# Optimization experiments

Hardware: AMD Instinct MI355X
Metric: run time of the kernel (lower is better)

Reference implementation:

```python
import jax, jax.numpy as jnp
import numpy as np

D_MODEL = 1024
NUM_HEADS = 16
ROPE_THETA = 10000.0


def setup_inputs() -> dict:
    key = jax.random.key(0)
    ks = jax.random.split(key, 5)
    B, S, D = 4, 2048, D_MODEL
    scale = 1.0 / np.sqrt(D)
    return {
        "x": jax.random.normal(ks[0], (B, S, D), dtype=jnp.float32),
        "Wq": jax.random.normal(ks[1], (D, D), dtype=jnp.float32) * scale,
        "Wk": jax.random.normal(ks[2], (D, D), dtype=jnp.float32) * scale,
        "Wv": jax.random.normal(ks[3], (D, D), dtype=jnp.float32) * scale,
        "Wo": jax.random.normal(ks[4], (D, D), dtype=jnp.float32) * scale,
        "token_positions": jnp.arange(S, dtype=jnp.int32),
    }


def _rope(x, pos, theta=ROPE_THETA):
    # x: (b, h, s, d); interleaved-pair rotary embedding
    d = x.shape[-1]
    inv_freq = 1.0 / (theta ** (jnp.arange(0, d, 2, dtype=jnp.float32) / d))  # (d/2,)
    ang = pos.astype(jnp.float32)[:, None] * inv_freq[None, :]  # (s, d/2)
    cos, sin = jnp.cos(ang), jnp.sin(ang)
    x1, x2 = x[..., ::2], x[..., 1::2]
    out = jnp.stack([x1 * cos - x2 * sin, x1 * sin + x2 * cos], axis=-1)
    return out.reshape(x.shape)


def reference(x, Wq, Wk, Wv, Wo, token_positions):
    B, S, D = x.shape
    H = NUM_HEADS
    dh = D // H
    # torch nn.Linear(bias=False): y = x @ W.T
    q = jnp.einsum('bsd,ed->bse', x, Wq).reshape(B, S, H, dh).transpose(0, 2, 1, 3)
    k = jnp.einsum('bsd,ed->bse', x, Wk).reshape(B, S, H, dh).transpose(0, 2, 1, 3)
    v = jnp.einsum('bsd,ed->bse', x, Wv).reshape(B, S, H, dh).transpose(0, 2, 1, 3)
    q = _rope(q, token_positions)
    k = _rope(k, token_positions)
    scores = jnp.einsum('bhqd,bhkd->bhqk', q, k) / jnp.sqrt(jnp.array(dh, x.dtype))
    causal = jnp.tril(jnp.ones((S, S), dtype=bool))
    scores = jnp.where(causal, scores, jnp.array(-jnp.inf, scores.dtype))
    probs = jax.nn.softmax(scores, axis=-1)
    attn = jnp.einsum('bhqk,bhkd->bhqd', probs, v)  # (b, h, s, dh)
    attn = attn.transpose(0, 2, 1, 3).reshape(B, S, D)
    return jnp.einsum('bsd,ed->bse', attn, Wo)
```

## Files before the change

### kernel.cpp

```cpp
#include <hip/hip_runtime.h>
#include <hip/hip_bf16.h>
#include <stdint.h>

#define S_LEN 2048
#define BATCH 4
#define NH    16
#define DH    64
#define DM    1024
#define MTOT  (BATCH*S_LEN)

typedef short bf16x8 __attribute__((ext_vector_type(8)));
typedef float f32x4 __attribute__((ext_vector_type(4)));
typedef uint32_t u32x4 __attribute__((ext_vector_type(4)));

__device__ __forceinline__ uint16_t f2bf(float f) {
  union { float f; uint32_t i; } c; c.f = f;
  uint32_t r = c.i + 0x7fffu + ((c.i >> 16) & 1u);
  return (uint16_t)(r >> 16);
}
__device__ __forceinline__ float bf2f(uint16_t u) {
  union { uint32_t i; float f; } c; c.i = ((uint32_t)u) << 16; return c.f;
}

__device__ __forceinline__ uint32_t cvt_pk_bf16(float a, float b) {
  uint32_t r;
  asm("v_cvt_pk_bf16_f32 %0, %1, %2" : "=v"(r) : "v"(a), "v"(b));
  return r;
}

__device__ __forceinline__ void async_copy16(void* lds, const void* g) {
  __builtin_amdgcn_global_load_lds(
      (const __attribute__((address_space(1))) void*)g,
      (__attribute__((address_space(3))) void*)lds, 16, 0, 0);
}

__global__ __launch_bounds__(256) void cvt_f32_bf16(const float* __restrict__ in,
                                                    uint16_t* __restrict__ out, int n4) {
  int stride = gridDim.x * blockDim.x;
  for (int i = blockIdx.x * blockDim.x + threadIdx.x; i < n4; i += stride) {
    float4 v = ((const float4*)in)[i];
    ushort4 o;
    o.x = f2bf(v.x); o.y = f2bf(v.y); o.z = f2bf(v.z); o.w = f2bf(v.w);
    ((ushort4*)out)[i] = o;
  }
}

__global__ __launch_bounds__(256) void cvt_w4(const float* __restrict__ wq,
                                              const float* __restrict__ wk,
                                              const float* __restrict__ wv,
                                              const float* __restrict__ wo,
                                              uint16_t* __restrict__ out) {
  const int sel = blockIdx.y;
  const float* src = sel == 0 ? wq : sel == 1 ? wk : sel == 2 ? wv : wo;
  uint16_t* dst = out + (size_t)sel * DM * DM;
  const int n4 = DM * DM / 4;
  const int stride = gridDim.x * blockDim.x;
  for (int i = blockIdx.x * blockDim.x + threadIdx.x; i < n4; i += stride) {
    float4 v = ((const float4*)src)[i];
    ushort4 o;
    o.x = f2bf(v.x); o.y = f2bf(v.y); o.z = f2bf(v.z); o.w = f2bf(v.w);
    ((ushort4*)dst)[i] = o;
  }
}

template<int MODE>
__global__ __launch_bounds__(256) void gemm_bt(const uint16_t* __restrict__ A,
                                               const uint16_t* __restrict__ Bw,
                                               void* __restrict__ outp) {
  constexpr int K = DM;
  constexpr int NT = K / 32;
  __shared__ __align__(16) uint16_t lA[3][128 * 32];
  __shared__ __align__(16) uint16_t lB[3][128 * 32];
  const int tid = threadIdx.x;
  const int w = tid >> 6, lane = tid & 63;
  const int l15 = lane & 15, lhi = lane >> 4;
  const int wr = w >> 1, wc = w & 1;

  const int nx = gridDim.x, nwg = nx * gridDim.y;
  const int flat = blockIdx.y * nx + blockIdx.x;
  const int wg = (flat & 7) * (nwg >> 3) + (flat >> 3);
  const int bm = (wg / nx) * 128, bn = (wg % nx) * 128;

  const int srow = tid >> 2;
  const int cb = (tid & 3) * 16;

  auto stage = [&](int b, int t) {
    const int k0 = t * 32;
#pragma unroll
    for (int i = 0; i < 2; ++i) {
      const int row = i * 64 + srow;
      async_copy16((char*)lA[b] + i * 4096 + w * 1024,
                   (const char*)A + ((size_t)(bm + row) * K + k0) * 2 + cb);
      async_copy16((char*)lB[b] + i * 4096 + w * 1024,
                   (const char*)Bw + ((size_t)(bn + row) * K + k0) * 2 + cb);
    }
  };

  f32x4 acc[4][4] = {};

  stage(0, 0);
  stage(1, 1);
  asm volatile("s_waitcnt vmcnt(4)" ::: "memory");
  __builtin_amdgcn_s_barrier();
  __builtin_amdgcn_sched_barrier(0);

  int cur = 0;
  for (int t = 0; t < NT; ++t) {
    const bool pre = (t + 2 < NT);
    int bnext = cur + 2; if (bnext >= 3) bnext -= 3;
    if (pre) stage(bnext, t + 2);

    bf16x8 af[4], bfr[4];
#pragma unroll
    for (int mf = 0; mf < 4; ++mf)
      af[mf] = *(const bf16x8*)((const char*)lA[cur] +
                                (wr * 64 + mf * 16 + l15) * 64 + lhi * 16);
#pragma unroll
    for (int nf = 0; nf < 4; ++nf)
      bfr[nf] = *(const bf16x8*)((const char*)lB[cur] +
                                 (wc * 64 + nf * 16 + l15) * 64 + lhi * 16);
    __builtin_amdgcn_s_setprio(1);
#pragma unroll
    for (int mf = 0; mf < 4; ++mf)
#pragma unroll
      for (int nf = 0; nf < 4; ++nf)
        acc[mf][nf] = __builtin_amdgcn_mfma_f32_16x16x32_bf16(af[mf], bfr[nf], acc[mf][nf], 0, 0, 0);
    __builtin_amdgcn_s_setprio(0);

    if (pre) asm volatile("s_waitcnt vmcnt(4)" ::: "memory");
    else     asm volatile("s_waitcnt vmcnt(0)" ::: "memory");
    __builtin_amdgcn_s_barrier();
    __builtin_amdgcn_sched_barrier(0);
    cur = cur + 1 == 3 ? 0 : cur + 1;
  }

  if (MODE == 0) {
    uint16_t* out = (uint16_t*)outp;
#pragma unroll
    for (int mf = 0; mf < 4; ++mf)
#pragma unroll
      for (int nf = 0; nf < 4; ++nf)
#pragma unroll
        for (int r = 0; r < 4; ++r) {
          const int m = bm + wr * 64 + mf * 16 + lhi * 4 + r;
          const int n = bn + wc * 64 + nf * 16 + l15;
          const int b = m >> 11, s = m & (S_LEN - 1);
          const int tsel = n >> 10, e = n & 1023;
          const int h = e >> 6, d = e & 63;
          out[(size_t)tsel * (MTOT * DM) +
              (((size_t)(b * NH + h) * S_LEN + s) << 6) + d] = f2bf(acc[mf][nf][r]);
        }
  } else {
    float* out = (float*)outp;
#pragma unroll
    for (int mf = 0; mf < 4; ++mf)
#pragma unroll
      for (int nf = 0; nf < 4; ++nf)
#pragma unroll
        for (int r = 0; r < 4; ++r) {
          const int m = bm + wr * 64 + mf * 16 + lhi * 4 + r;
          const int n = bn + wc * 64 + nf * 16 + l15;
          out[(size_t)m * DM + n] = acc[mf][nf][r];
        }
  }
}

__global__ __launch_bounds__(256) void rope_kernel(uint32_t* __restrict__ q,
                                                   uint32_t* __restrict__ k,
                                                   const int* __restrict__ pos) {
  const int total = BATCH * NH * S_LEN * 32;
  const float l2t = 13.287712379549449f;
  const float qsc = 0.18033688011112042f;
  const int stride = gridDim.x * blockDim.x;
  for (int idx = blockIdx.x * blockDim.x + threadIdx.x; idx < total; idx += stride) {
    const int i = idx & 31;
    const int s = (idx >> 5) & (S_LEN - 1);
    const float p = (float)pos[s];
    const float inv = __builtin_amdgcn_exp2f(-(float)i * (l2t * (1.0f / 32.0f)));
    const float ang = p * inv;
    const float sn = sinf(ang), cs = cosf(ang);
    {
      uint32_t u = q[idx];
      float x1 = bf2f((uint16_t)(u & 0xffffu));
      float x2 = bf2f((uint16_t)(u >> 16));
      q[idx] = (uint32_t)f2bf((x1 * cs - x2 * sn) * qsc) |
               ((uint32_t)f2bf((x1 * sn + x2 * cs) * qsc) << 16);
    }
    {
      uint32_t u = k[idx];
      float x1 = bf2f((uint16_t)(u & 0xffffu));
      float x2 = bf2f((uint16_t)(u >> 16));
      k[idx] = (uint32_t)f2bf(x1 * cs - x2 * sn) | ((uint32_t)f2bf(x1 * sn + x2 * cs) << 16);
    }
  }
}

__global__ __launch_bounds__(256) void transpose_v(const uint16_t* __restrict__ v,
                                                   uint16_t* __restrict__ vt) {
  __shared__ uint16_t t[64 * 65];
  const int bh = blockIdx.y, s0 = blockIdx.x * 64;
  const uint16_t* vb = v + (size_t)bh * S_LEN * 64 + (size_t)s0 * 64;
  uint16_t* ob = vt + (size_t)bh * 64 * S_LEN + s0;
  for (int o = threadIdx.x; o < 64 * 64; o += 256) {
    const int r = o >> 6, c = o & 63;
    t[c * 65 + r] = vb[(size_t)r * 64 + c];
  }
  __syncthreads();
  for (int o = threadIdx.x; o < 64 * 64; o += 256) {
    const int d = o >> 6, p = o & 63;
    const int sp = (p & 32) | (((p >> 2) & 3) << 3) | (((p >> 4) & 1) << 2) | (p & 3);
    ob[(size_t)d * S_LEN + sp] = t[d * 65 + p];
  }
}

__global__ __launch_bounds__(512, 4) void attn_kernel(const uint16_t* __restrict__ q,
                                                      const uint16_t* __restrict__ kk,
                                                      const uint16_t* __restrict__ vt,
                                                      uint16_t* __restrict__ o) {
  const int bh = blockIdx.y;
  const int p = blockIdx.x;
  const int tid = threadIdx.x;
  const int w = __builtin_amdgcn_readfirstlane(tid >> 6);
  const int lane = tid & 63;
  const int l15 = lane & 15, lhi = lane >> 4;
  const uint16_t* qb = q + (size_t)bh * S_LEN * DH;
  const uint16_t* kb = kk + (size_t)bh * S_LEN * DH;
  const uint16_t* vb = vt + (size_t)bh * DH * S_LEN;

  __shared__ uint16_t lK[2][128 * 64];
  __shared__ uint16_t lV[2][64 * 128];

  const int krow_l = lane >> 3;
  const int scK = (lane & 7) ^ krow_l;
  const int vrow_l = lane >> 4;

  auto stage = [&](int b, int t) {
    const int k0 = t * 128;
#pragma unroll
    for (int i = 0; i < 2; ++i) {
      const int krow = w * 16 + i * 8 + krow_l;
      async_copy16((char*)lK[b] + w * 2048 + i * 1024 + lane * 16,
                   (const char*)kb + ((size_t)(k0 + krow) * 64 + scK * 8) * 2);
      const int vd = w * 8 + i * 4 + vrow_l;
      const int scV = (lane & 15) ^ (vd & 15);
      async_copy16((char*)lV[b] + w * 2048 + i * 1024 + lane * 16,
                   (const char*)vb + ((size_t)vd * S_LEN + k0 + scV * 8) * 2);
    }
  };

  stage(0, 0);
  asm volatile("s_waitcnt vmcnt(0)" ::: "memory");
  __syncthreads();

  int cur = 0;
  const int b_out = bh >> 4, h_out = bh & 15;

  for (int s = 0; s < 2; ++s) {
    const int qtile = s ? p : (15 - p);
    const int q0 = qtile * 128 + w * 16;

    bf16x8 qf[2];
#pragma unroll
    for (int c = 0; c < 2; ++c)
      qf[c] = *(const bf16x8*)(qb + (size_t)(q0 + l15) * DH + c * 32 + lhi * 8);

    f32x4 oa[4] = {};
    float mr = -1e30f, lr = 0.f;

    const int nt = qtile + 1;
    for (int t = 0; t < nt; ++t) {
      if (t + 1 < nt) stage(cur ^ 1, t + 1);
      else if (s == 0) stage(cur ^ 1, 0);

      const bool diag = (t == qtile);
      const int fMf = diag ? w : 7;
      const int fE  = diag ? (w | 1) : 7;
      const int cE  = diag ? (w >> 1) : 3;

      f32x4 sf[8];
      __builtin_amdgcn_s_setprio(1);
#pragma unroll
      for (int f = 0; f < 8; ++f) {
        f32x4 z = {0.f, 0.f, 0.f, 0.f};
        if (f <= fMf) {
          const int kr = f * 16 + l15;
          const char* kbase = (const char*)lK[cur] + kr * 128;
          bf16x8 kf0 = *(const bf16x8*)(kbase + ((lhi ^ (kr & 7)) << 4));
          bf16x8 kf1 = *(const bf16x8*)(kbase + (((4 + lhi) ^ (kr & 7)) << 4));
          z = __builtin_amdgcn_mfma_f32_16x16x32_bf16(kf0, qf[0], z, 0, 0, 0);
          z = __builtin_amdgcn_mfma_f32_16x16x32_bf16(kf1, qf[1], z, 0, 0, 0);
        }
        sf[f] = z;
      }
      __builtin_amdgcn_s_setprio(0);

      if (diag) {
        const int qrow = q0 + l15;
        const int k0 = t * 128;
#pragma unroll
        for (int f = 0; f < 8; ++f)
          if (f <= fE)
#pragma unroll
            for (int r = 0; r < 4; ++r) {
              const int kv = k0 + f * 16 + lhi * 4 + r;
              if (kv > qrow) sf[f][r] = -1e30f;
            }
      }

      float pm = -1e30f;
#pragma unroll
      for (int f = 0; f < 8; ++f)
        if (f <= fE)
#pragma unroll
          for (int r = 0; r < 4; ++r) pm = fmaxf(pm, sf[f][r]);
      pm = fmaxf(pm, __shfl_xor(pm, 16));
      pm = fmaxf(pm, __shfl_xor(pm, 32));

      if (!__all(pm <= mr + 8.0f)) {
        const float mn = fmaxf(mr, pm);
        const float resc = __builtin_amdgcn_exp2f(mr - mn);
        mr = mn;
        lr *= resc;
#pragma unroll
        for (int r = 0; r < 4; ++r) {
          const float rb = __shfl(resc, (lhi << 2) + r);
#pragma unroll
          for (int df = 0; df < 4; ++df) oa[df][r] *= rb;
        }
      }

      float rs = 0.f;
#pragma unroll
      for (int f = 0; f < 8; ++f)
        if (f <= fE)
#pragma unroll
          for (int r = 0; r < 4; ++r) {
            const float pv = __builtin_amdgcn_exp2f(sf[f][r] - mr);
            sf[f][r] = pv;
            rs += pv;
          }
      rs += __shfl_xor(rs, 16);
      rs += __shfl_xor(rs, 32);
      lr += rs;

#pragma unroll
      for (int c = 0; c < 4; ++c) {
        if (c <= cE) {
          u32x4 u;
          u.x = cvt_pk_bf16(sf[2 * c][0], sf[2 * c][1]);
          u.y = cvt_pk_bf16(sf[2 * c][2], sf[2 * c][3]);
          u.z = cvt_pk_bf16(sf[2 * c + 1][0], sf[2 * c + 1][1]);
          u.w = cvt_pk_bf16(sf[2 * c + 1][2], sf[2 * c + 1][3]);
          bf16x8 pa = __builtin_bit_cast(bf16x8, u);
          __builtin_amdgcn_s_setprio(1);
#pragma unroll
          for (int df = 0; df < 4; ++df) {
            const int vr = df * 16 + l15;
            bf16x8 vf = *(const bf16x8*)((const char*)lV[cur] + vr * 256 +
                                         ((((c << 2) + lhi) ^ (vr & 15)) << 4));
            oa[df] = __builtin_amdgcn_mfma_f32_16x16x32_bf16(pa, vf, oa[df], 0, 0, 0);
          }
          __builtin_amdgcn_s_setprio(0);
        }
      }

      asm volatile("s_waitcnt vmcnt(0)" ::: "memory");
      __syncthreads();
      cur ^= 1;
    }

    float inv[4];
#pragma unroll
    for (int r = 0; r < 4; ++r)
      inv[r] = __builtin_amdgcn_rcpf(__shfl(lr, (lhi << 2) + r));
#pragma unroll
    for (int df = 0; df < 4; ++df)
#pragma unroll
      for (int r = 0; r < 4; ++r) {
        const int srow_o = q0 + lhi * 4 + r;
        const float val = oa[df][r] * inv[r];
        const int d = df * 16 + l15;
        o[((size_t)(b_out * S_LEN + srow_o)) * DM + h_out * 64 + d] = f2bf(val);
      }
  }
}

extern "C" void kernel_launch(void* const* d_in, const int* in_sizes, int n_in,
                              void* d_out, int out_size, void* d_ws, size_t ws_size,
                              hipStream_t stream) {
  const float* x = (const float*)d_in[0];
  const float* Wq = (const float*)d_in[1];
  const float* Wk = (const float*)d_in[2];
  const float* Wv = (const float*)d_in[3];
  const float* Wo = (const float*)d_in[4];
  const int* pos = (const int*)d_in[5];

  char* ws = (char*)d_ws;
  size_t off = 0;
  auto alloc = [&](size_t bytes) {
    void* p = ws + off;
    off += (bytes + 255) & ~(size_t)255;
    return p;
  };
  uint16_t* xb    = (uint16_t*)alloc((size_t)MTOT * DM * 2);
  uint16_t* wqkvb = (uint16_t*)alloc((size_t)4 * DM * DM * 2);
  uint16_t* qkvb  = (uint16_t*)alloc((size_t)3 * MTOT * DM * 2);
  uint16_t* vtb   = (uint16_t*)alloc((size_t)MTOT * DM * 2);
  uint16_t* wob = wqkvb + (size_t)3 * DM * DM;
  uint16_t* qb = qkvb;
  uint16_t* kbuf = qkvb + (size_t)MTOT * DM;
  uint16_t* vbuf = qkvb + (size_t)2 * MTOT * DM;
  uint16_t* attnb = xb;

  cvt_f32_bf16<<<2048, 256, 0, stream>>>(x, xb, MTOT * DM / 4);
  cvt_w4<<<dim3(128, 4), 256, 0, stream>>>(Wq, Wk, Wv, Wo, wqkvb);

  gemm_bt<0><<<dim3(24, MTOT / 128), 256, 0, stream>>>(xb, wqkvb, qkvb);

  rope_kernel<<<2048, 256, 0, stream>>>((uint32_t*)qb, (uint32_t*)kbuf, pos);
  transpose_v<<<dim3(32, 64), 256, 0, stream>>>(vbuf, vtb);

  attn_kernel<<<dim3(8, 64), 512, 0, stream>>>(qb, kbuf, vtb, attnb);

  gemm_bt<1><<<dim3(8, MTOT / 128), 256, 0, stream>>>(attnb, wob, d_out);
}
```

Baseline: 187.5 us.

## Fuse RoPE into QKV GEMM epilogue and narrow output-projection tile

RoPE rotation and the query scaling now happen in the QKV GEMM epilogue. Each lane takes its pair element from a neighbour lane with a shuffle, which removes the separate rope kernel and its extra read-modify-write of Q and K. The GEMM is templated on the N tile width. The output projection uses BN=64, doubling its workgroup count from 512 to 1024 for better CU occupancy. The risks are per-element transcendental cost in the epilogue (__sinf/__cosf instead of sinf/cosf, lower accuracy at large angles) and less reuse per tile in the narrower projection GEMM.

```diff
diff --git a/kernel.cpp b/kernel.cpp
--- a/kernel.cpp
+++ b/kernel.cpp
@@ -63,14 +63,17 @@
   }
 }
 
-template<int MODE>
+template<int MODE, int BN>
 __global__ __launch_bounds__(256) void gemm_bt(const uint16_t* __restrict__ A,
                                                const uint16_t* __restrict__ Bw,
-                                               void* __restrict__ outp) {
+                                               void* __restrict__ outp,
+                                               const int* __restrict__ pos) {
   constexpr int K = DM;
   constexpr int NT = K / 32;
+  constexpr int WC = BN / 2;
+  constexpr int NF = WC / 16;
   __shared__ __align__(16) uint16_t lA[3][128 * 32];
-  __shared__ __align__(16) uint16_t lB[3][128 * 32];
+  __shared__ __align__(16) uint16_t lB[3][BN * 32];
   const int tid = threadIdx.x;
   const int w = tid >> 6, lane = tid & 63;
   const int l15 = lane & 15, lhi = lane >> 4;
@@ -79,7 +82,7 @@
   const int nx = gridDim.x, nwg = nx * gridDim.y;
   const int flat = blockIdx.y * nx + blockIdx.x;
   const int wg = (flat & 7) * (nwg >> 3) + (flat >> 3);
-  const int bm = (wg / nx) * 128, bn = (wg % nx) * 128;
+  const int bm = (wg / nx) * 128, bn = (wg % nx) * BN;
 
   const int srow = tid >> 2;
   const int cb = (tid & 3) * 16;
@@ -87,20 +90,21 @@
   auto stage = [&](int b, int t) {
     const int k0 = t * 32;
 #pragma unroll
-    for (int i = 0; i < 2; ++i) {
-      const int row = i * 64 + srow;
+    for (int i = 0; i < 2; ++i)
       async_copy16((char*)lA[b] + i * 4096 + w * 1024,
-                   (const char*)A + ((size_t)(bm + row) * K + k0) * 2 + cb);
+                   (const char*)A + ((size_t)(bm + i * 64 + srow) * K + k0) * 2 + cb);
+#pragma unroll
+    for (int i = 0; i < BN / 64; ++i)
       async_copy16((char*)lB[b] + i * 4096 + w * 1024,
-                   (const char*)Bw + ((size_t)(bn + row) * K + k0) * 2 + cb);
-    }
+                   (const char*)Bw + ((size_t)(bn + i * 64 + srow) * K + k0) * 2 + cb);
   };
 
-  f32x4 acc[4][4] = {};
+  f32x4 acc[4][NF] = {};
 
   stage(0, 0);
   stage(1, 1);
-  asm volatile("s_waitcnt vmcnt(4)" ::: "memory");
+  if constexpr (BN == 128) asm volatile("s_waitcnt vmcnt(4)" ::: "memory");
+  else                     asm volatile("s_waitcnt vmcnt(3)" ::: "memory");
   __builtin_amdgcn_s_barrier();
   __builtin_amdgcn_sched_barrier(0);
 
@@ -110,88 +114,94 @@
     int bnext = cur + 2; if (bnext >= 3) bnext -= 3;
     if (pre) stage(bnext, t + 2);
 
-    bf16x8 af[4], bfr[4];
+    bf16x8 af[4], bfr[NF];
 #pragma unroll
     for (int mf = 0; mf < 4; ++mf)
       af[mf] = *(const bf16x8*)((const char*)lA[cur] +
                                 (wr * 64 + mf * 16 + l15) * 64 + lhi * 16);
 #pragma unroll
-    for (int nf = 0; nf < 4; ++nf)
+    for (int nf = 0; nf < NF; ++nf)
       bfr[nf] = *(const bf16x8*)((const char*)lB[cur] +
-                                 (wc * 64 + nf * 16 + l15) * 64 + lhi * 16);
+                                 (wc * WC + nf * 16 + l15) * 64 + lhi * 16);
     __builtin_amdgcn_s_setprio(1);
 #pragma unroll
     for (int mf = 0; mf < 4; ++mf)
 #pragma unroll
-      for (int nf = 0; nf < 4; ++nf)
+      for (int nf = 0; nf < NF; ++nf)
         acc[mf][nf] = __builtin_amdgcn_mfma_f32_16x16x32_bf16(af[mf], bfr[nf], acc[mf][nf], 0, 0, 0);
     __builtin_amdgcn_s_setprio(0);
 
-    if (pre) asm volatile("s_waitcnt vmcnt(4)" ::: "memory");
-    else     asm volatile("s_waitcnt vmcnt(0)" ::: "memory");
+    if (pre) {
+      if constexpr (BN == 128) asm volatile("s_waitcnt vmcnt(4)" ::: "memory");
+      else                     asm volatile("s_waitcnt vmcnt(3)" ::: "memory");
+    } else {
+      asm volatile("s_waitcnt vmcnt(0)" ::: "memory");
+    }
     __builtin_amdgcn_s_barrier();
     __builtin_amdgcn_sched_barrier(0);
     cur = cur + 1 == 3 ? 0 : cur + 1;
   }
 
   if (MODE == 0) {
-    uint16_t* out = (uint16_t*)outp;
-#pragma unroll
-    for (int mf = 0; mf < 4; ++mf)
-#pragma unroll
-      for (int nf = 0; nf < 4; ++nf)
+    const int tsel = bn >> 10;
+    uint16_t* out = (uint16_t*)outp + (size_t)tsel * ((size_t)MTOT * DM);
+    if (tsel < 2) {
+      const float l2t_32 = 0.41524101186092074f;
+      const float qsc = tsel == 0 ? 0.18033688011112042f : 1.0f;
+#pragma unroll
+      for (int mf = 0; mf < 4; ++mf) {
+        float ps[4];
 #pragma unroll
         for (int r = 0; r < 4; ++r) {
           const int m = bm + wr * 64 + mf * 16 + lhi * 4 + r;
-          const int n = bn + wc * 64 + nf * 16 + l15;
-          const int b = m >> 11, s = m & (S_LEN - 1);
-          const int tsel = n >> 10, e = n & 1023;
+          ps[r] = (float)pos[m & (S_LEN - 1)];
+        }
+#pragma unroll
+        for (int nf = 0; nf < NF; ++nf) {
+          const int n = bn + wc * WC + nf * 16 + l15;
+          const int e = n & 1023;
           const int h = e >> 6, d = e & 63;
-          out[(size_t)tsel * (MTOT * DM) +
-              (((size_t)(b * NH + h) * S_LEN + s) << 6) + d] = f2bf(acc[mf][nf][r]);
-        }
+          const float inv = __builtin_amdgcn_exp2f(-(float)(d >> 1) * l2t_32);
+#pragma unroll
+          for (int r = 0; r < 4; ++r) {
+            const int m = bm + wr * 64 + mf * 16 + lhi * 4 + r;
+            const int b = m >> 11, s = m & (S_LEN - 1);
+            const float v = acc[mf][nf][r];
+            const float p = __shfl_xor(v, 1);
+            const float ang = ps[r] * inv;
+            const float cs = __cosf(ang) * qsc, sn = __sinf(ang) * qsc;
+            const float val = (l15 & 1) ? (p * sn + v * cs) : (v * cs - p * sn);
+            out[(((size_t)(b * NH + h) * S_LEN + s) << 6) + d] = f2bf(val);
+          }
+        }
+      }
+    } else {
+#pragma unroll
+      for (int mf = 0; mf < 4; ++mf)
+#pragma unroll
+        for (int nf = 0; nf < NF; ++nf)
+#pragma unroll
+          for (int r = 0; r < 4; ++r) {
+            const int m = bm + wr * 64 + mf * 16 + lhi * 4 + r;
+            const int n = bn + wc * WC + nf * 16 + l15;
+            const int b = m >> 11, s = m & (S_LEN - 1);
+            const int e = n & 1023;
+            const int h = e >> 6, d = e & 63;
+            out[(((size_t)(b * NH + h) * S_LEN + s) << 6) + d] = f2bf(acc[mf][nf][r]);
+          }
+    }
   } else {
     float* out = (float*)outp;
 #pragma unroll
     for (int mf = 0; mf < 4; ++mf)
 #pragma unroll
-      for (int nf = 0; nf < 4; ++nf)
+      for (int nf = 0; nf < NF; ++nf)
 #pragma unroll
         for (int r = 0; r < 4; ++r) {
           const int m = bm + wr * 64 + mf * 16 + lhi * 4 + r;
-          const int n = bn + wc * 64 + nf * 16 + l15;
+          const int n = bn + wc * WC + nf * 16 + l15;
           out[(size_t)m * DM + n] = acc[mf][nf][r];
         }
-  }
-}
-
-__global__ __launch_bounds__(256) void rope_kernel(uint32_t* __restrict__ q,
-                                                   uint32_t* __restrict__ k,
-                                                   const int* __restrict__ pos) {
-  const int total = BATCH * NH * S_LEN * 32;
-  const float l2t = 13.287712379549449f;
-  const float qsc = 0.18033688011112042f;
-  const int stride = gridDim.x * blockDim.x;
-  for (int idx = blockIdx.x * blockDim.x + threadIdx.x; idx < total; idx += stride) {
-    const int i = idx & 31;
-    const int s = (idx >> 5) & (S_LEN - 1);
-    const float p = (float)pos[s];
-    const float inv = __builtin_amdgcn_exp2f(-(float)i * (l2t * (1.0f / 32.0f)));
-    const float ang = p * inv;
-    const float sn = sinf(ang), cs = cosf(ang);
-    {
-      uint32_t u = q[idx];
-      float x1 = bf2f((uint16_t)(u & 0xffffu));
-      float x2 = bf2f((uint16_t)(u >> 16));
-      q[idx] = (uint32_t)f2bf((x1 * cs - x2 * sn) * qsc) |
-               ((uint32_t)f2bf((x1 * sn + x2 * cs) * qsc) << 16);
-    }
-    {
-      uint32_t u = k[idx];
-      float x1 = bf2f((uint16_t)(u & 0xffffu));
-      float x2 = bf2f((uint16_t)(u >> 16));
-      k[idx] = (uint32_t)f2bf(x1 * cs - x2 * sn) | ((uint32_t)f2bf(x1 * sn + x2 * cs) << 16);
-    }
   }
 }
 
@@ -415,12 +425,11 @@
   cvt_f32_bf16<<<2048, 256, 0, stream>>>(x, xb, MTOT * DM / 4);
   cvt_w4<<<dim3(128, 4), 256, 0, stream>>>(Wq, Wk, Wv, Wo, wqkvb);
 
-  gemm_bt<0><<<dim3(24, MTOT / 128), 256, 0, stream>>>(xb, wqkvb, qkvb);
-
-  rope_kernel<<<2048, 256, 0, stream>>>((uint32_t*)qb, (uint32_t*)kbuf, pos);
+  gemm_bt<0, 128><<<dim3(24, MTOT / 128), 256, 0, stream>>>(xb, wqkvb, qkvb, pos);
+
   transpose_v<<<dim3(32, 64), 256, 0, stream>>>(vbuf, vtb);
 
   attn_kernel<<<dim3(8, 64), 512, 0, stream>>>(qb, kbuf, vtb, attnb);
 
-  gemm_bt<1><<<dim3(8, MTOT / 128), 256, 0, stream>>>(attnb, wob, d_out);
-}
+  gemm_bt<1, 64><<<dim3(16, MTOT / 128), 256, 0, stream>>>(attnb, wob, d_out, nullptr);
+}
```

New measurement: 176.4 us. 1.06x faster.
